# Kernel optimization log

Hardware: AMD Instinct MI355X
Metric: run time of the kernel (lower is better)

Reference implementation:

```python
import jax, jax.numpy as jnp
import numpy as np

B, T, V, H, E, MAX_OOV = 128, 200, 50257, 256, 128, 50


def setup_inputs() -> dict:
    key = jax.random.key(0)
    ks = jax.random.split(key, 17)
    s = 0.05  # param scale
    return {
        "decoder_input": jax.random.randint(ks[0], (B, 1), 0, V),
        "encoder_outputs": jax.random.normal(ks[1], (B, T, 2 * H), jnp.float32),
        "encoder_idxs": jax.random.randint(ks[2], (B, T), 0, V),
        "prev_state": jax.random.normal(ks[3], (1, B, H), jnp.float32),
        "selective_read": jax.random.normal(ks[4], (B, 1, 2 * H), jnp.float32) * s,
        "step": 1,
        "emb": jax.random.normal(ks[5], (V, E), jnp.float32) * s,
        "W_ih": jax.random.normal(ks[6], (3 * H, E + 2 * H), jnp.float32) * s,
        "W_hh": jax.random.normal(ks[7], (3 * H, H), jnp.float32) * s,
        "b_ih": jax.random.normal(ks[8], (3 * H,), jnp.float32) * s,
        "b_hh": jax.random.normal(ks[9], (3 * H,), jnp.float32) * s,
        "Wi_w": jax.random.normal(ks[10], (H, 2 * H), jnp.float32) * s,
        "Wi_b": jax.random.normal(ks[11], (H,), jnp.float32) * s,
        "Wg_w": jax.random.normal(ks[12], (V, H), jnp.float32) * s,
        "Wg_b": jax.random.normal(ks[13], (V,), jnp.float32) * s,
        "Wc_w": jax.random.normal(ks[14], (H, 2 * H), jnp.float32) * s,
        "Wc_b": jax.random.normal(ks[15], (H,), jnp.float32) * s,
    }


def _gru_cell(x, h, W_ih, W_hh, b_ih, b_hh):
    # torch GRUCell math, gate order r,z,n
    gi = x @ W_ih.T + b_ih
    gh = h @ W_hh.T + b_hh
    i_r, i_z, i_n = jnp.split(gi, 3, axis=-1)
    h_r, h_z, h_n = jnp.split(gh, 3, axis=-1)
    r = jax.nn.sigmoid(i_r + h_r)
    z = jax.nn.sigmoid(i_z + h_z)
    n = jnp.tanh(i_n + r * h_n)
    return (1.0 - z) * n + z * h


def reference(decoder_input, encoder_outputs, encoder_idxs, prev_state, selective_read,
              step, emb, W_ih, W_hh, b_ih, b_hh, Wi_w, Wi_b, Wg_w, Wg_b, Wc_w, Wc_b):
    dtype = encoder_outputs.dtype
    if step == 0:
        prev_state = (encoder_outputs[:, -1] @ Wi_w.T + Wi_b)[None]      # 1,B,H
        selective_read = jnp.zeros((B, 1, 2 * H), dtype)
    embedded = emb[decoder_input[:, 0]]                                   # B,E
    gru_in = jnp.concatenate([selective_read[:, 0], embedded], axis=-1)   # B,2H+E
    decode_hidden = _gru_cell(gru_in, prev_state[0], W_ih, W_hh, b_ih, b_hh)  # B,H

    score_g = decode_hidden @ Wg_w.T + Wg_b                               # B,V
    enc_proj = jnp.tanh(jnp.einsum('bte,he->bth', encoder_outputs, Wc_w) + Wc_b)  # B,T,H
    score_c = jnp.tanh(jnp.einsum('bth,bh->bt', enc_proj, decode_hidden))         # B,T
    score_c = score_c + jnp.where(encoder_idxs == 0, -10000.0, 0.0).astype(dtype)

    probs = jax.nn.softmax(jnp.concatenate([score_g, score_c], axis=1), axis=1)   # B,V+T
    prob_g, prob_c = probs[:, :V], probs[:, V:]
    prob_g = jnp.concatenate([prob_g, jnp.full((B, MAX_OOV), 1e-4, dtype)], axis=1)  # B,V+oov

    # copy-distribution aggregation: scatter-add prob_c by vocab id (replaces one-hot bmm)
    prob_c_to_g = jnp.zeros((B, V + MAX_OOV), dtype).at[
        jnp.arange(B)[:, None], encoder_idxs].add(prob_c)
    prob_out = (prob_c_to_g + prob_g)[:, None, :]                          # B,1,V+oov

    # selective read for next step
    match = (encoder_idxs == decoder_input).astype(dtype)                  # B,T
    tot = match.sum(axis=1, keepdims=True)
    match = jnp.where(tot > 1, match / tot, match)
    prob_appeared = prob_c * match
    selective_read_new = jnp.einsum('bt,bte->be', prob_appeared, encoder_outputs)[:, None, :]  # B,1,2H
    return prob_out, decode_hidden, selective_read_new
```

## Files before the change

### kernel.cpp

```cpp
#include <hip/hip_runtime.h>

typedef __bf16 bf16;
typedef __bf16 bf16x4 __attribute__((ext_vector_type(4)));
typedef __bf16 bf16x8 __attribute__((ext_vector_type(8)));
typedef float f32x4 __attribute__((ext_vector_type(4)));

#define B_ 128
#define T_ 200
#define V_ 50257
#define H_ 256
#define E_ 128
#define OOV_ 50
#define VO_ 50307
#define NRG 80
#define NTS 5
#define GSC 629
#define PSTR 640
#define GPJ 400

__device__ __forceinline__ float sigmoid_(float x) { return 1.0f / (1.0f + __expf(-x)); }
__device__ __forceinline__ float tanh_(float x) { return 1.0f - 2.0f / (__expf(2.0f * x) + 1.0f); }

__global__ void k_front(const float* Wc_w, bf16* WcPack,
                        const int* step_p, const float* enc, const float* prev,
                        const float* selread, const int* dec, const float* emb,
                        const float* Wi_w, const float* Wi_b,
                        float* hT, float* ginT) {
    if (blockIdx.x < 128) {
        int gid = blockIdx.x * 256 + threadIdx.x;
        int n = gid >> 7;
        int k = (gid & 127) * 4;
        float4 v = *(const float4*)(Wc_w + n * 512 + k);
        int kstep = k >> 5, kin = k & 31;
        int q = kin >> 3, j0 = kin & 7;
        int r = n & 15, nt = n >> 4;
        int lane = q * 16 + r;
        bf16* d = WcPack + (((nt * 16 + kstep) * 64) + lane) * 8 + j0;
        d[0] = (bf16)v.x; d[1] = (bf16)v.y; d[2] = (bf16)v.z; d[3] = (bf16)v.w;
    } else {
        int b = blockIdx.x - 128, t = threadIdx.x;
        int step = step_p[0];
        float h;
        if (step == 0) {
            float acc = Wi_b[t];
            const float* er = enc + (b * T_ + (T_ - 1)) * 512;
            const float* wr = Wi_w + t * 512;
            for (int k = 0; k < 512; ++k) acc += er[k] * wr[k];
            h = acc;
        } else {
            h = prev[b * H_ + t];
        }
        hT[t * B_ + b] = h;
        for (int k = t; k < 512; k += 256)
            ginT[k * B_ + b] = (step == 0) ? 0.0f : selread[b * 512 + k];
        if (t < E_)
            ginT[(512 + t) * B_ + b] = emb[dec[b] * E_ + t];
    }
}

__global__ void k_gemm_gru(const float* W_ih, const float* b_ih,
                           const float* W_hh, const float* b_hh,
                           const float* ginT, const float* hT,
                           float* giT, float* ghT) {
    __shared__ float red[256];
    int rrow = blockIdx.x;
    int t = threadIdx.x;
    int b = t & 127, kh = t >> 7;
    const float* w = W_ih + rrow * 640 + kh * 320;
    const float* g = ginT + (kh * 320) * B_ + b;
    float a0 = 0.f, a1 = 0.f, a2 = 0.f, a3 = 0.f;
#pragma unroll 4
    for (int k = 0; k < 320; k += 4) {
        a0 += w[k]     * g[k * B_];
        a1 += w[k + 1] * g[(k + 1) * B_];
        a2 += w[k + 2] * g[(k + 2) * B_];
        a3 += w[k + 3] * g[(k + 3) * B_];
    }
    const float* w2 = W_hh + rrow * 256 + kh * 128;
    const float* hh = hT + (kh * 128) * B_ + b;
    float c0 = 0.f, c1 = 0.f, c2 = 0.f, c3 = 0.f;
#pragma unroll 4
    for (int k = 0; k < 128; k += 4) {
        c0 += w2[k]     * hh[k * B_];
        c1 += w2[k + 1] * hh[(k + 1) * B_];
        c2 += w2[k + 2] * hh[(k + 2) * B_];
        c3 += w2[k + 3] * hh[(k + 3) * B_];
    }
    red[t] = ((a0 + a1) + (a2 + a3));
    __syncthreads();
    if (kh == 0) giT[rrow * B_ + b] = b_ih[rrow] + red[b] + red[b + 128];
    __syncthreads();
    red[t] = ((c0 + c1) + (c2 + c3));
    __syncthreads();
    if (kh == 0) ghT[rrow * B_ + b] = b_hh[rrow] + red[b] + red[b + 128];
}

__global__ void k_gru_cell(const float* giT, const float* ghT, const float* hT,
                           float* out_dh, bf16* Apack) {
    int b = blockIdx.x, j = threadIdx.x;
    float ir = giT[j * B_ + b], iz = giT[(256 + j) * B_ + b], in_ = giT[(512 + j) * B_ + b];
    float hr = ghT[j * B_ + b], hz = ghT[(256 + j) * B_ + b], hn = ghT[(512 + j) * B_ + b];
    float hp = hT[j * B_ + b];
    float r = sigmoid_(ir + hr);
    float z = sigmoid_(iz + hz);
    float n = tanh_(in_ + r * hn);
    float h = (1.0f - z) * n + z * hp;
    out_dh[b * H_ + j] = h;
    int mt = b >> 4, rr = b & 15, ks = j >> 5, q = (j >> 3) & 3, jj = j & 7;
    Apack[(((mt * 8 + ks) * 64) + (q * 16 + rr)) * 8 + jj] = (bf16)h;
}

__global__ __launch_bounds__(256, 3) void k_mm(const bf16* Apack, const float* Wg_w,
                                               const float* Wg_b, const float* enc,
                                               const bf16* WcPack, const float* Wc_b,
                                               const float* dh, const int* idxs,
                                               float* out_prob, float* pg_part, float* expc) {
    __shared__ unsigned char smem[34816];
    int tid = threadIdx.x;
    int w = tid >> 6, lane = tid & 63;
    int r = lane & 15, q = lane >> 4;
    if (blockIdx.x < GSC) {
        int blk = blockIdx.x;
        int n0 = blk * NRG;
        const float* rp[NTS];
        bool valid[NTS];
        int nrow[NTS];
#pragma unroll
        for (int nt = 0; nt < NTS; ++nt) {
            int n = n0 + nt * 16 + r;
            valid[nt] = (n < V_);
            nrow[nt] = valid[nt] ? n : (V_ - 1);
            rp[nt] = Wg_w + nrow[nt] * 256 + q * 8;
        }
        f32x4 acc[10];
#pragma unroll
        for (int i = 0; i < 10; ++i) acc[i] = (f32x4){0.f, 0.f, 0.f, 0.f};
        float4 vA[NTS], vB[NTS];
#pragma unroll
        for (int nt = 0; nt < NTS; ++nt) {
            vA[nt] = *(const float4*)(rp[nt]);
            vB[nt] = *(const float4*)(rp[nt] + 4);
        }
#pragma unroll
        for (int ks = 0; ks < 8; ++ks) {
            bf16x8 bfr[NTS];
#pragma unroll
            for (int nt = 0; nt < NTS; ++nt) {
                float4 va = vA[nt], vb = vB[nt];
                bfr[nt][0] = (bf16)va.x; bfr[nt][1] = (bf16)va.y;
                bfr[nt][2] = (bf16)va.z; bfr[nt][3] = (bf16)va.w;
                bfr[nt][4] = (bf16)vb.x; bfr[nt][5] = (bf16)vb.y;
                bfr[nt][6] = (bf16)vb.z; bfr[nt][7] = (bf16)vb.w;
            }
            if (ks < 7) {
#pragma unroll
                for (int nt = 0; nt < NTS; ++nt) {
                    vA[nt] = *(const float4*)(rp[nt] + (ks + 1) * 32);
                    vB[nt] = *(const float4*)(rp[nt] + (ks + 1) * 32 + 4);
                }
            }
            bf16x8 a0 = *(const bf16x8*)(Apack + ((2 * w + 0) * 8 + ks) * 512 + lane * 8);
            bf16x8 a1 = *(const bf16x8*)(Apack + ((2 * w + 1) * 8 + ks) * 512 + lane * 8);
#pragma unroll
            for (int nt = 0; nt < NTS; ++nt) {
                acc[nt * 2]     = __builtin_amdgcn_mfma_f32_16x16x32_bf16(a0, bfr[nt], acc[nt * 2], 0, 0, 0);
                acc[nt * 2 + 1] = __builtin_amdgcn_mfma_f32_16x16x32_bf16(a1, bfr[nt], acc[nt * 2 + 1], 0, 0, 0);
            }
        }
        float rsum[2][4];
#pragma unroll
        for (int p = 0; p < 2; ++p)
#pragma unroll
            for (int rg = 0; rg < 4; ++rg) rsum[p][rg] = 0.0f;
#pragma unroll
        for (int nt = 0; nt < NTS; ++nt) {
            float wgb = Wg_b[nrow[nt]];
            int n = n0 + nt * 16 + r;
#pragma unroll
            for (int p = 0; p < 2; ++p) {
#pragma unroll
                for (int rg = 0; rg < 4; ++rg) {
                    int row = (2 * w + p) * 16 + q * 4 + rg;
                    float e = valid[nt] ? __expf(acc[nt * 2 + p][rg] + wgb) : 0.0f;
                    rsum[p][rg] += e;
                    if (valid[nt]) out_prob[row * VO_ + n] = e;
                }
            }
        }
#pragma unroll
        for (int p = 0; p < 2; ++p) {
#pragma unroll
            for (int rg = 0; rg < 4; ++rg) {
                float s = rsum[p][rg];
                s += __shfl_xor(s, 1);
                s += __shfl_xor(s, 2);
                s += __shfl_xor(s, 4);
                s += __shfl_xor(s, 8);
                if (r == 0) {
                    int row = (2 * w + p) * 16 + q * 4 + rg;
                    pg_part[row * PSTR + blk] = s;
                }
            }
        }
    } else {
        int pblk = blockIdx.x - GSC;
        int m0 = pblk * 64;
        bf16* As = (bf16*)smem;
        float* sred = (float*)(smem + 33792);
        f32x4 acc[16];
#pragma unroll
        for (int i = 0; i < 16; ++i) acc[i] = (f32x4){0.f, 0.f, 0.f, 0.f};
        for (int half = 0; half < 2; ++half) {
            __syncthreads();
#pragma unroll
            for (int ph = 0; ph < 2; ++ph) {
                float4 tmp[8];
#pragma unroll
                for (int j = 0; j < 8; ++j) {
                    int f = (ph * 8 + j) * 256 + tid;
                    int row = f >> 6, c4 = f & 63;
                    tmp[j] = *(const float4*)(enc + (m0 + row) * 512 + half * 256 + c4 * 4);
                }
#pragma unroll
                for (int j = 0; j < 8; ++j) {
                    int f = (ph * 8 + j) * 256 + tid;
                    int row = f >> 6, c4 = f & 63;
                    bf16x4 o;
                    o[0] = (bf16)tmp[j].x; o[1] = (bf16)tmp[j].y;
                    o[2] = (bf16)tmp[j].z; o[3] = (bf16)tmp[j].w;
                    *(bf16x4*)(As + row * 264 + c4 * 4) = o;
                }
            }
            __syncthreads();
#pragma unroll
            for (int ks = 0; ks < 8; ++ks) {
                int kstep = half * 8 + ks;
                bf16x8 bfr[4];
#pragma unroll
                for (int ntl = 0; ntl < 4; ++ntl)
                    bfr[ntl] = *(const bf16x8*)(WcPack + (((w * 4 + ntl) * 16 + kstep) * 64 + lane) * 8);
#pragma unroll
                for (int mt = 0; mt < 4; ++mt) {
                    bf16x8 a = *(const bf16x8*)(As + (mt * 16 + r) * 264 + ks * 32 + q * 8);
#pragma unroll
                    for (int ntl = 0; ntl < 4; ++ntl)
                        acc[mt * 4 + ntl] = __builtin_amdgcn_mfma_f32_16x16x32_bf16(a, bfr[ntl], acc[mt * 4 + ntl], 0, 0, 0);
                }
            }
        }
#pragma unroll
        for (int mt = 0; mt < 4; ++mt) {
#pragma unroll
            for (int rg = 0; rg < 4; ++rg) {
                int rowl = mt * 16 + q * 4 + rg;
                int row = m0 + rowl;
                int b = row / T_;
                float s = 0.0f;
#pragma unroll
                for (int ntl = 0; ntl < 4; ++ntl) {
                    int n = (w * 4 + ntl) * 16 + r;
                    float pv = tanh_(acc[mt * 4 + ntl][rg] + Wc_b[n]);
                    s += pv * dh[b * H_ + n];
                }
                s += __shfl_xor(s, 1);
                s += __shfl_xor(s, 2);
                s += __shfl_xor(s, 4);
                s += __shfl_xor(s, 8);
                if (r == 0) sred[rowl * 4 + w] = s;
            }
        }
        __syncthreads();
        if (tid < 64) {
            float s = sred[tid * 4] + sred[tid * 4 + 1] + sred[tid * 4 + 2] + sred[tid * 4 + 3];
            int row = m0 + tid;
            int b = row / T_, t = row - b * T_;
            float sc = tanh_(s);
            if (idxs[b * T_ + t] == 0) sc -= 10000.0f;
            expc[row] = __expf(sc);
        }
    }
}

__global__ void k_red_scatter(const float* pg_part, const float* expc_, const int* idxs,
                              const int* dec, const float* enc,
                              float* out_prob, float* out_sel) {
    __shared__ float red[256];
    __shared__ float cf[256];
    int b = blockIdx.x >> 1, hf = blockIdx.x & 1;
    int t = threadIdx.x;
    float s = 0.0f;
    for (int i = t; i < GSC; i += 256) s += pg_part[b * PSTR + i];
    if (t < T_) s += expc_[b * T_ + t];
    red[t] = s;
    __syncthreads();
    for (int k = 128; k > 0; k >>= 1) {
        if (t < k) red[t] += red[t + k];
        __syncthreads();
    }
    float iv = 1.0f / red[0];
    __syncthreads();
    int d = dec[b];
    const int halfc = (VO_ + 1) / 2;
    int cl0 = hf * halfc;
    int cl1 = (cl0 + halfc < VO_) ? cl0 + halfc : VO_;
    float ec = 0.0f;
    int m = 0;
    if (t < T_) {
        int ix = idxs[b * T_ + t];
        ec = expc_[b * T_ + t];
        if (ix >= cl0 && ix < cl1)
            atomicAdd(&out_prob[b * VO_ + ix], ec);
        m = (ix == d) ? 1 : 0;
    }
    cf[t] = m ? ec * iv : 0.0f;
    red[t] = m ? 1.0f : 0.0f;
    __syncthreads();
    for (int k = 128; k > 0; k >>= 1) {
        if (t < k) red[t] += red[t + k];
        __syncthreads();
    }
    float tot = red[0];
    float scale = (tot > 1.0f) ? 1.0f / tot : 1.0f;
    int dim = t + hf * 256;
    float a0 = 0.0f;
    for (int tt = 0; tt < T_; ++tt) {
        float c = cf[tt];
        if (c != 0.0f) a0 += c * scale * enc[(b * T_ + tt) * 512 + dim];
    }
    out_sel[b * 512 + dim] = a0;
    __threadfence();
    __syncthreads();
    int base = b * VO_;
    int s0 = base + cl0, s1 = base + cl1;
    int a4 = (s0 + 3) & ~3;
    int b4 = s1 & ~3;
    if (t < a4 - s0) {
        int i = s0 + t;
        int col = i - base;
        out_prob[i] = (col < V_) ? out_prob[i] * iv : 1e-4f;
    }
    if (t < s1 - b4) {
        int i = b4 + t;
        int col = i - base;
        out_prob[i] = (col < V_) ? out_prob[i] * iv : 1e-4f;
    }
    for (int i4 = a4 / 4 + t; i4 < b4 / 4; i4 += 256) {
        float4 v = *(const float4*)(out_prob + i4 * 4);
        int c0 = i4 * 4 - base;
        float o[4];
        o[0] = (c0 + 0 < V_) ? v.x * iv : 1e-4f;
        o[1] = (c0 + 1 < V_) ? v.y * iv : 1e-4f;
        o[2] = (c0 + 2 < V_) ? v.z * iv : 1e-4f;
        o[3] = (c0 + 3 < V_) ? v.w * iv : 1e-4f;
        *(float4*)(out_prob + i4 * 4) = make_float4(o[0], o[1], o[2], o[3]);
    }
}

extern "C" void kernel_launch(void* const* d_in, const int* in_sizes, int n_in,
                              void* d_out, int out_size, void* d_ws, size_t ws_size,
                              hipStream_t stream) {
    const int*   dec     = (const int*)d_in[0];
    const float* enc     = (const float*)d_in[1];
    const int*   idxs    = (const int*)d_in[2];
    const float* prev    = (const float*)d_in[3];
    const float* selread = (const float*)d_in[4];
    const int*   step_p  = (const int*)d_in[5];
    const float* emb     = (const float*)d_in[6];
    const float* W_ih    = (const float*)d_in[7];
    const float* W_hh    = (const float*)d_in[8];
    const float* b_ih    = (const float*)d_in[9];
    const float* b_hh    = (const float*)d_in[10];
    const float* Wi_w    = (const float*)d_in[11];
    const float* Wi_b    = (const float*)d_in[12];
    const float* Wg_w    = (const float*)d_in[13];
    const float* Wg_b    = (const float*)d_in[14];
    const float* Wc_w    = (const float*)d_in[15];
    const float* Wc_b    = (const float*)d_in[16];

    float* ws     = (float*)d_ws;
    float* hT     = ws;
    float* ginT   = ws + 32768;
    float* giT    = ws + 114688;
    float* ghT    = ws + 212992;
    float* expc   = ws + 311552;
    float* pgp    = ws + 337152;
    bf16*  Apack  = (bf16*)(ws + 741376);
    bf16*  WcPack = (bf16*)(ws + 757760);

    float* out      = (float*)d_out;
    float* out_prob = out;
    float* out_dh   = out + 6439296;
    float* out_sel  = out + 6439296 + 32768;

    k_front<<<256, 256, 0, stream>>>(Wc_w, WcPack, step_p, enc, prev, selread, dec,
                                     emb, Wi_w, Wi_b, hT, ginT);
    k_gemm_gru<<<768, 256, 0, stream>>>(W_ih, b_ih, W_hh, b_hh, ginT, hT, giT, ghT);
    k_gru_cell<<<B_, 256, 0, stream>>>(giT, ghT, hT, out_dh, Apack);
    k_mm<<<GSC + GPJ, 256, 0, stream>>>(Apack, Wg_w, Wg_b, enc, WcPack, Wc_b,
                                        out_dh, idxs, out_prob, pgp, expc);
    k_red_scatter<<<256, 256, 0, stream>>>(pgp, expc, idxs, dec, enc, out_prob, out_sel);
}
```

Measured before the change: 279.6 us.

## Stage exp scores in bf16 workspace and split score/projection kernels

Generation-score exponentials are now written as bf16 into a workspace instead of fp32 into the output. The finish kernel reads that buffer, normalizes it and writes the output in a single pass. This removes one full fp32 read-modify-write of the large probability tensor. The fused score/projection kernel is split into two launches, and the score kernel is retiled to 512 threads with 64 columns per block. The copy scatter-add now runs after normalization with pre-scaled values. The costs are bf16 rounding of the probabilities and the loss of the explicit prefetch of weight loads.

```diff
diff --git a/kernel.cpp b/kernel.cpp
--- a/kernel.cpp
+++ b/kernel.cpp
@@ -12,10 +12,11 @@
 #define E_ 128
 #define OOV_ 50
 #define VO_ 50307
-#define NRG 80
-#define NTS 5
-#define GSC 629
-#define PSTR 640
+#define NRG 64
+#define NTS 4
+#define GSC 786
+#define PSTR 800
+#define PBSTR 50368
 #define GPJ 400
 
 __device__ __forceinline__ float sigmoid_(float x) { return 1.0f / (1.0f + __expf(-x)); }
@@ -110,180 +111,155 @@
     Apack[(((mt * 8 + ks) * 64) + (q * 16 + rr)) * 8 + jj] = (bf16)h;
 }
 
-__global__ __launch_bounds__(256, 3) void k_mm(const bf16* Apack, const float* Wg_w,
-                                               const float* Wg_b, const float* enc,
-                                               const bf16* WcPack, const float* Wc_b,
-                                               const float* dh, const int* idxs,
-                                               float* out_prob, float* pg_part, float* expc) {
+__global__ __launch_bounds__(512, 6) void k_score(const bf16* Apack, const float* Wg_w,
+                                                  const float* Wg_b,
+                                                  bf16* expg, float* pg_part) {
+    int tid = threadIdx.x;
+    int w = tid >> 6, lane = tid & 63;
+    int r = lane & 15, q = lane >> 4;
+    int blk = blockIdx.x;
+    int n0 = blk * NRG;
+    int off[NTS];
+#pragma unroll
+    for (int nt = 0; nt < NTS; ++nt) {
+        int n = n0 + nt * 16 + r;
+        off[nt] = ((n < V_) ? n : (V_ - 1)) * 256;
+    }
+    const float* bp = Wg_w + q * 8;
+    f32x4 acc[NTS];
+#pragma unroll
+    for (int i = 0; i < NTS; ++i) acc[i] = (f32x4){0.f, 0.f, 0.f, 0.f};
+#pragma unroll
+    for (int ks = 0; ks < 8; ++ks) {
+        bf16x8 a = *(const bf16x8*)(Apack + (w * 8 + ks) * 512 + lane * 8);
+        bf16x8 bfr[NTS];
+#pragma unroll
+        for (int nt = 0; nt < NTS; ++nt) {
+            float4 va = *(const float4*)(bp + off[nt] + ks * 32);
+            float4 vb = *(const float4*)(bp + off[nt] + ks * 32 + 4);
+            bfr[nt][0] = (bf16)va.x; bfr[nt][1] = (bf16)va.y;
+            bfr[nt][2] = (bf16)va.z; bfr[nt][3] = (bf16)va.w;
+            bfr[nt][4] = (bf16)vb.x; bfr[nt][5] = (bf16)vb.y;
+            bfr[nt][6] = (bf16)vb.z; bfr[nt][7] = (bf16)vb.w;
+        }
+#pragma unroll
+        for (int nt = 0; nt < NTS; ++nt)
+            acc[nt] = __builtin_amdgcn_mfma_f32_16x16x32_bf16(a, bfr[nt], acc[nt], 0, 0, 0);
+    }
+    float rsum[4] = {0.f, 0.f, 0.f, 0.f};
+#pragma unroll
+    for (int nt = 0; nt < NTS; ++nt) {
+        int n = n0 + nt * 16 + r;
+        bool valid = (n < V_);
+        float wgb = Wg_b[valid ? n : (V_ - 1)];
+#pragma unroll
+        for (int rg = 0; rg < 4; ++rg) {
+            int row = w * 16 + q * 4 + rg;
+            float e = valid ? __expf(acc[nt][rg] + wgb) : 0.0f;
+            rsum[rg] += e;
+            expg[row * PBSTR + n] = (bf16)e;
+        }
+    }
+#pragma unroll
+    for (int rg = 0; rg < 4; ++rg) {
+        float s = rsum[rg];
+        s += __shfl_xor(s, 1);
+        s += __shfl_xor(s, 2);
+        s += __shfl_xor(s, 4);
+        s += __shfl_xor(s, 8);
+        if (r == 0) {
+            int row = w * 16 + q * 4 + rg;
+            pg_part[row * PSTR + blk] = s;
+        }
+    }
+}
+
+__global__ __launch_bounds__(256, 4) void k_proj(const float* enc, const bf16* WcPack,
+                                                 const float* Wc_b, const float* dh,
+                                                 const int* idxs, float* expc) {
     __shared__ unsigned char smem[34816];
     int tid = threadIdx.x;
     int w = tid >> 6, lane = tid & 63;
     int r = lane & 15, q = lane >> 4;
-    if (blockIdx.x < GSC) {
-        int blk = blockIdx.x;
-        int n0 = blk * NRG;
-        const float* rp[NTS];
-        bool valid[NTS];
-        int nrow[NTS];
-#pragma unroll
-        for (int nt = 0; nt < NTS; ++nt) {
-            int n = n0 + nt * 16 + r;
-            valid[nt] = (n < V_);
-            nrow[nt] = valid[nt] ? n : (V_ - 1);
-            rp[nt] = Wg_w + nrow[nt] * 256 + q * 8;
-        }
-        f32x4 acc[10];
-#pragma unroll
-        for (int i = 0; i < 10; ++i) acc[i] = (f32x4){0.f, 0.f, 0.f, 0.f};
-        float4 vA[NTS], vB[NTS];
-#pragma unroll
-        for (int nt = 0; nt < NTS; ++nt) {
-            vA[nt] = *(const float4*)(rp[nt]);
-            vB[nt] = *(const float4*)(rp[nt] + 4);
-        }
+    int m0 = blockIdx.x * 64;
+    bf16* As = (bf16*)smem;
+    float* sred = (float*)(smem + 33792);
+    f32x4 acc[16];
+#pragma unroll
+    for (int i = 0; i < 16; ++i) acc[i] = (f32x4){0.f, 0.f, 0.f, 0.f};
+    for (int half = 0; half < 2; ++half) {
+        __syncthreads();
+#pragma unroll
+        for (int ph = 0; ph < 2; ++ph) {
+            float4 tmp[8];
+#pragma unroll
+            for (int j = 0; j < 8; ++j) {
+                int f = (ph * 8 + j) * 256 + tid;
+                int row = f >> 6, c4 = f & 63;
+                tmp[j] = *(const float4*)(enc + (m0 + row) * 512 + half * 256 + c4 * 4);
+            }
+#pragma unroll
+            for (int j = 0; j < 8; ++j) {
+                int f = (ph * 8 + j) * 256 + tid;
+                int row = f >> 6, c4 = f & 63;
+                bf16x4 o;
+                o[0] = (bf16)tmp[j].x; o[1] = (bf16)tmp[j].y;
+                o[2] = (bf16)tmp[j].z; o[3] = (bf16)tmp[j].w;
+                *(bf16x4*)(As + row * 264 + c4 * 4) = o;
+            }
+        }
+        __syncthreads();
 #pragma unroll
         for (int ks = 0; ks < 8; ++ks) {
-            bf16x8 bfr[NTS];
-#pragma unroll
-            for (int nt = 0; nt < NTS; ++nt) {
-                float4 va = vA[nt], vb = vB[nt];
-                bfr[nt][0] = (bf16)va.x; bfr[nt][1] = (bf16)va.y;
-                bfr[nt][2] = (bf16)va.z; bfr[nt][3] = (bf16)va.w;
-                bfr[nt][4] = (bf16)vb.x; bfr[nt][5] = (bf16)vb.y;
-                bfr[nt][6] = (bf16)vb.z; bfr[nt][7] = (bf16)vb.w;
+            int kstep = half * 8 + ks;
+            bf16x8 bfr[4];
+#pragma unroll
+            for (int ntl = 0; ntl < 4; ++ntl)
+                bfr[ntl] = *(const bf16x8*)(WcPack + (((w * 4 + ntl) * 16 + kstep) * 64 + lane) * 8);
+#pragma unroll
+            for (int mt = 0; mt < 4; ++mt) {
+                bf16x8 a = *(const bf16x8*)(As + (mt * 16 + r) * 264 + ks * 32 + q * 8);
+#pragma unroll
+                for (int ntl = 0; ntl < 4; ++ntl)
+                    acc[mt * 4 + ntl] = __builtin_amdgcn_mfma_f32_16x16x32_bf16(a, bfr[ntl], acc[mt * 4 + ntl], 0, 0, 0);
             }
-            if (ks < 7) {
-#pragma unroll
-                for (int nt = 0; nt < NTS; ++nt) {
-                    vA[nt] = *(const float4*)(rp[nt] + (ks + 1) * 32);
-                    vB[nt] = *(const float4*)(rp[nt] + (ks + 1) * 32 + 4);
-                }
+        }
+    }
+#pragma unroll
+    for (int mt = 0; mt < 4; ++mt) {
+#pragma unroll
+        for (int rg = 0; rg < 4; ++rg) {
+            int rowl = mt * 16 + q * 4 + rg;
+            int row = m0 + rowl;
+            int b = row / T_;
+            float s = 0.0f;
+#pragma unroll
+            for (int ntl = 0; ntl < 4; ++ntl) {
+                int n = (w * 4 + ntl) * 16 + r;
+                float pv = tanh_(acc[mt * 4 + ntl][rg] + Wc_b[n]);
+                s += pv * dh[b * H_ + n];
             }
-            bf16x8 a0 = *(const bf16x8*)(Apack + ((2 * w + 0) * 8 + ks) * 512 + lane * 8);
-            bf16x8 a1 = *(const bf16x8*)(Apack + ((2 * w + 1) * 8 + ks) * 512 + lane * 8);
-#pragma unroll
-            for (int nt = 0; nt < NTS; ++nt) {
-                acc[nt * 2]     = __builtin_amdgcn_mfma_f32_16x16x32_bf16(a0, bfr[nt], acc[nt * 2], 0, 0, 0);
-                acc[nt * 2 + 1] = __builtin_amdgcn_mfma_f32_16x16x32_bf16(a1, bfr[nt], acc[nt * 2 + 1], 0, 0, 0);
-            }
-        }
-        float rsum[2][4];
-#pragma unroll
-        for (int p = 0; p < 2; ++p)
-#pragma unroll
-            for (int rg = 0; rg < 4; ++rg) rsum[p][rg] = 0.0f;
-#pragma unroll
-        for (int nt = 0; nt < NTS; ++nt) {
-            float wgb = Wg_b[nrow[nt]];
-            int n = n0 + nt * 16 + r;
-#pragma unroll
-            for (int p = 0; p < 2; ++p) {
-#pragma unroll
-                for (int rg = 0; rg < 4; ++rg) {
-                    int row = (2 * w + p) * 16 + q * 4 + rg;
-                    float e = valid[nt] ? __expf(acc[nt * 2 + p][rg] + wgb) : 0.0f;
-                    rsum[p][rg] += e;
-                    if (valid[nt]) out_prob[row * VO_ + n] = e;
-                }
-            }
-        }
-#pragma unroll
-        for (int p = 0; p < 2; ++p) {
-#pragma unroll
-            for (int rg = 0; rg < 4; ++rg) {
-                float s = rsum[p][rg];
-                s += __shfl_xor(s, 1);
-                s += __shfl_xor(s, 2);
-                s += __shfl_xor(s, 4);
-                s += __shfl_xor(s, 8);
-                if (r == 0) {
-                    int row = (2 * w + p) * 16 + q * 4 + rg;
-                    pg_part[row * PSTR + blk] = s;
-                }
-            }
-        }
-    } else {
-        int pblk = blockIdx.x - GSC;
-        int m0 = pblk * 64;
-        bf16* As = (bf16*)smem;
-        float* sred = (float*)(smem + 33792);
-        f32x4 acc[16];
-#pragma unroll
-        for (int i = 0; i < 16; ++i) acc[i] = (f32x4){0.f, 0.f, 0.f, 0.f};
-        for (int half = 0; half < 2; ++half) {
-            __syncthreads();
-#pragma unroll
-            for (int ph = 0; ph < 2; ++ph) {
-                float4 tmp[8];
-#pragma unroll
-                for (int j = 0; j < 8; ++j) {
-                    int f = (ph * 8 + j) * 256 + tid;
-                    int row = f >> 6, c4 = f & 63;
-                    tmp[j] = *(const float4*)(enc + (m0 + row) * 512 + half * 256 + c4 * 4);
-                }
-#pragma unroll
-                for (int j = 0; j < 8; ++j) {
-                    int f = (ph * 8 + j) * 256 + tid;
-                    int row = f >> 6, c4 = f & 63;
-                    bf16x4 o;
-                    o[0] = (bf16)tmp[j].x; o[1] = (bf16)tmp[j].y;
-                    o[2] = (bf16)tmp[j].z; o[3] = (bf16)tmp[j].w;
-                    *(bf16x4*)(As + row * 264 + c4 * 4) = o;
-                }
-            }
-            __syncthreads();
-#pragma unroll
-            for (int ks = 0; ks < 8; ++ks) {
-                int kstep = half * 8 + ks;
-                bf16x8 bfr[4];
-#pragma unroll
-                for (int ntl = 0; ntl < 4; ++ntl)
-                    bfr[ntl] = *(const bf16x8*)(WcPack + (((w * 4 + ntl) * 16 + kstep) * 64 + lane) * 8);
-#pragma unroll
-                for (int mt = 0; mt < 4; ++mt) {
-                    bf16x8 a = *(const bf16x8*)(As + (mt * 16 + r) * 264 + ks * 32 + q * 8);
-#pragma unroll
-                    for (int ntl = 0; ntl < 4; ++ntl)
-                        acc[mt * 4 + ntl] = __builtin_amdgcn_mfma_f32_16x16x32_bf16(a, bfr[ntl], acc[mt * 4 + ntl], 0, 0, 0);
-                }
-            }
-        }
-#pragma unroll
-        for (int mt = 0; mt < 4; ++mt) {
-#pragma unroll
-            for (int rg = 0; rg < 4; ++rg) {
-                int rowl = mt * 16 + q * 4 + rg;
-                int row = m0 + rowl;
-                int b = row / T_;
-                float s = 0.0f;
-#pragma unroll
-                for (int ntl = 0; ntl < 4; ++ntl) {
-                    int n = (w * 4 + ntl) * 16 + r;
-                    float pv = tanh_(acc[mt * 4 + ntl][rg] + Wc_b[n]);
-                    s += pv * dh[b * H_ + n];
-                }
-                s += __shfl_xor(s, 1);
-                s += __shfl_xor(s, 2);
-                s += __shfl_xor(s, 4);
-                s += __shfl_xor(s, 8);
-                if (r == 0) sred[rowl * 4 + w] = s;
-            }
-        }
-        __syncthreads();
-        if (tid < 64) {
-            float s = sred[tid * 4] + sred[tid * 4 + 1] + sred[tid * 4 + 2] + sred[tid * 4 + 3];
-            int row = m0 + tid;
-            int b = row / T_, t = row - b * T_;
-            float sc = tanh_(s);
-            if (idxs[b * T_ + t] == 0) sc -= 10000.0f;
-            expc[row] = __expf(sc);
-        }
-    }
-}
-
-__global__ void k_red_scatter(const float* pg_part, const float* expc_, const int* idxs,
-                              const int* dec, const float* enc,
-                              float* out_prob, float* out_sel) {
+            s += __shfl_xor(s, 1);
+            s += __shfl_xor(s, 2);
+            s += __shfl_xor(s, 4);
+            s += __shfl_xor(s, 8);
+            if (r == 0) sred[rowl * 4 + w] = s;
+        }
+    }
+    __syncthreads();
+    if (tid < 64) {
+        float s = sred[tid * 4] + sred[tid * 4 + 1] + sred[tid * 4 + 2] + sred[tid * 4 + 3];
+        int row = m0 + tid;
+        int b = row / T_, t = row - b * T_;
+        float sc = tanh_(s);
+        if (idxs[b * T_ + t] == 0) sc -= 10000.0f;
+        expc[row] = __expf(sc);
+    }
+}
+
+__global__ void k_finish(const float* pg_part, const float* expc_, const int* idxs,
+                         const int* dec, const float* enc, const bf16* expg,
+                         float* out_prob, float* out_sel) {
     __shared__ float red[256];
     __shared__ float cf[256];
     int b = blockIdx.x >> 1, hf = blockIdx.x & 1;
@@ -300,16 +276,12 @@
     float iv = 1.0f / red[0];
     __syncthreads();
     int d = dec[b];
-    const int halfc = (VO_ + 1) / 2;
-    int cl0 = hf * halfc;
-    int cl1 = (cl0 + halfc < VO_) ? cl0 + halfc : VO_;
     float ec = 0.0f;
+    int ix = -1;
     int m = 0;
     if (t < T_) {
-        int ix = idxs[b * T_ + t];
+        ix = idxs[b * T_ + t];
         ec = expc_[b * T_ + t];
-        if (ix >= cl0 && ix < cl1)
-            atomicAdd(&out_prob[b * VO_ + ix], ec);
         m = (ix == d) ? 1 : 0;
     }
     cf[t] = m ? ec * iv : 0.0f;
@@ -328,32 +300,38 @@
         if (c != 0.0f) a0 += c * scale * enc[(b * T_ + tt) * 512 + dim];
     }
     out_sel[b * 512 + dim] = a0;
-    __threadfence();
-    __syncthreads();
+    const int halfc = (VO_ + 1) / 2;
+    int cl0 = hf * halfc;
+    int cl1 = (cl0 + halfc < VO_) ? cl0 + halfc : VO_;
     int base = b * VO_;
+    const bf16* eg = expg + b * PBSTR;
     int s0 = base + cl0, s1 = base + cl1;
     int a4 = (s0 + 3) & ~3;
     int b4 = s1 & ~3;
     if (t < a4 - s0) {
         int i = s0 + t;
         int col = i - base;
-        out_prob[i] = (col < V_) ? out_prob[i] * iv : 1e-4f;
+        out_prob[i] = (col < V_) ? (float)eg[col] * iv : 1e-4f;
     }
     if (t < s1 - b4) {
         int i = b4 + t;
         int col = i - base;
-        out_prob[i] = (col < V_) ? out_prob[i] * iv : 1e-4f;
+        out_prob[i] = (col < V_) ? (float)eg[col] * iv : 1e-4f;
     }
     for (int i4 = a4 / 4 + t; i4 < b4 / 4; i4 += 256) {
-        float4 v = *(const float4*)(out_prob + i4 * 4);
         int c0 = i4 * 4 - base;
         float o[4];
-        o[0] = (c0 + 0 < V_) ? v.x * iv : 1e-4f;
-        o[1] = (c0 + 1 < V_) ? v.y * iv : 1e-4f;
-        o[2] = (c0 + 2 < V_) ? v.z * iv : 1e-4f;
-        o[3] = (c0 + 3 < V_) ? v.w * iv : 1e-4f;
+#pragma unroll
+        for (int c = 0; c < 4; ++c) {
+            int col = c0 + c;
+            o[c] = (col < V_) ? (float)eg[col] * iv : 1e-4f;
+        }
         *(float4*)(out_prob + i4 * 4) = make_float4(o[0], o[1], o[2], o[3]);
     }
+    __threadfence();
+    __syncthreads();
+    if (t < T_ && ix >= cl0 && ix < cl1)
+        atomicAdd(&out_prob[base + ix], ec * iv);
 }
 
 extern "C" void kernel_launch(void* const* d_in, const int* in_sizes, int n_in,
@@ -386,6 +364,7 @@
     float* pgp    = ws + 337152;
     bf16*  Apack  = (bf16*)(ws + 741376);
     bf16*  WcPack = (bf16*)(ws + 757760);
+    bf16*  expg   = (bf16*)(ws + 823296);
 
     float* out      = (float*)d_out;
     float* out_prob = out;
@@ -396,7 +375,7 @@
                                      emb, Wi_w, Wi_b, hT, ginT);
     k_gemm_gru<<<768, 256, 0, stream>>>(W_ih, b_ih, W_hh, b_hh, ginT, hT, giT, ghT);
     k_gru_cell<<<B_, 256, 0, stream>>>(giT, ghT, hT, out_dh, Apack);
-    k_mm<<<GSC + GPJ, 256, 0, stream>>>(Apack, Wg_w, Wg_b, enc, WcPack, Wc_b,
-                                        out_dh, idxs, out_prob, pgp, expc);
-    k_red_scatter<<<256, 256, 0, stream>>>(pgp, expc, idxs, dec, enc, out_prob, out_sel);
-}
+    k_proj<<<GPJ, 256, 0, stream>>>(enc, WcPack, Wc_b, out_dh, idxs, expc);
+    k_score<<<GSC, 512, 0, stream>>>(Apack, Wg_w, Wg_b, expg, pgp);
+    k_finish<<<256, 256, 0, stream>>>(pgp, expc, idxs, dec, enc, expg, out_prob, out_sel);
+}
```

New measurement: 348.9 us. 24.8% more time.
